# Kernel tuning notes

Measured on AMD Instinct MI355X. Metric: run time of the kernel, lower is better.

Reference implementation:

```python
import jax, jax.numpy as jnp
import numpy as np

HEAD_DIM = 128
NUM_BUCKETS = 32
MAX_DISTANCE = 128


def _rel_pos_bucket(seq_len):
    # T5 causal relative-position bucketing (lucidrains flash-pytorch version)
    pos = jnp.arange(seq_len)
    rel = pos[None, :] - pos[:, None]          # k_pos - q_pos
    n = jnp.maximum(-rel, 0)                   # causal: only past distances
    max_exact = NUM_BUCKETS // 2
    is_small = n < max_exact
    n_safe = jnp.maximum(n, 1).astype(jnp.float32)
    val_large = max_exact + (
        jnp.log(n_safe / max_exact) / np.log(MAX_DISTANCE / max_exact)
        * (NUM_BUCKETS - max_exact)
    ).astype(jnp.int32)
    val_large = jnp.minimum(val_large, NUM_BUCKETS - 1)
    return jnp.where(is_small, n, val_large)   # (S, S) int32


def setup_inputs() -> dict:
    key = jax.random.key(0)
    ks = jax.random.split(key, 10)
    B, S, D, I = 4, 2048, 768, 1536
    s = 0.02
    return {
        "x": jax.random.normal(ks[0], (B, S, D), jnp.float32),
        "v_W": jax.random.normal(ks[1], (D, I), jnp.float32) * s,
        "v_b": jnp.zeros((I,), jnp.float32),
        "g_W": jax.random.normal(ks[2], (D, I), jnp.float32) * s,
        "g_b": jnp.zeros((I,), jnp.float32),
        "in_W": jax.random.normal(ks[3], (D, HEAD_DIM), jnp.float32) * s,
        "in_b": jnp.zeros((HEAD_DIM,), jnp.float32),
        "q_gamma": jax.random.normal(ks[4], (HEAD_DIM,), jnp.float32) * s,
        "q_beta": jnp.zeros((HEAD_DIM,), jnp.float32),
        "k_gamma": jax.random.normal(ks[5], (HEAD_DIM,), jnp.float32) * s,
        "k_beta": jnp.zeros((HEAD_DIM,), jnp.float32),
        "out_W": jax.random.normal(ks[6], (I, D), jnp.float32) * s,
        "out_b": jnp.zeros((D,), jnp.float32),
        "rel_emb": jax.random.normal(ks[7], (NUM_BUCKETS, 1), jnp.float32) * s,
    }


def reference(x, v_W, v_b, g_W, g_b, in_W, in_b,
              q_gamma, q_beta, k_gamma, k_beta, out_W, out_b, rel_emb):
    silu = jax.nn.silu
    S = x.shape[1]
    v = silu(x @ v_W + v_b)                    # (B, S, I)
    gate = silu(x @ g_W + g_b)                 # (B, S, I)
    base = silu(x @ in_W + in_b)               # (B, S, 128)
    q = base * q_gamma + q_beta
    k = base * k_gamma + k_beta
    # scores scaled by sqrt(v dim) per torch code (v.size(-1) = inner_dim)
    attn = jnp.einsum('bns,bms->bnm', q, k) / jnp.sqrt(jnp.float32(v.shape[-1]))
    bias = rel_emb[_rel_pos_bucket(S), 0] * np.sqrt(HEAD_DIM)  # (S, S)
    attn = attn + bias
    causal = jnp.triu(jnp.ones((S, S), bool), 1)
    attn = jnp.where(causal, 0.0, attn)        # masked_fill to 0 before relu^2
    attn = jnp.square(jax.nn.relu(attn))       # ReLU^2 attention (no softmax)
    o = jnp.einsum('bnm,bme->bne', attn, v) * gate
    return o @ out_W + out_b                   # (B, S, D)
```

## Files before the change

### kernel.cpp

```cpp
#include <hip/hip_runtime.h>


typedef short short8 __attribute__((ext_vector_type(8)));
typedef float f32x4 __attribute__((ext_vector_type(4)));
typedef unsigned short us4 __attribute__((ext_vector_type(4)));
typedef float fl4 __attribute__((ext_vector_type(4)));

#define BM 128
#define BN 128
#define BK 64

enum { EPI_VT = 0, EPI_GQK = 1, EPI_SCORES = 3, EPI_OUT = 5 };

__device__ __forceinline__ unsigned short f2bf(float f) {
  unsigned u = __builtin_bit_cast(unsigned, f);
  u += 0x7FFFu + ((u >> 16) & 1u);
  return (unsigned short)(u >> 16);
}
__device__ __forceinline__ float bf2f(unsigned short b) {
  return __builtin_bit_cast(float, ((unsigned)b) << 16);
}
__device__ __forceinline__ float silu_f(float x) { return x / (1.0f + __expf(-x)); }

__device__ __forceinline__ void gl_lds(const unsigned short* gp, unsigned short* lp) {
  __builtin_amdgcn_global_load_lds((const __attribute__((address_space(1))) void*)gp,
                                   (__attribute__((address_space(3))) void*)lp, 16, 0, 0);
}

__device__ __forceinline__ void stage_tile(const unsigned short* __restrict__ g,
                                           int row_stride, int r0, int ko,
                                           unsigned short* lds, int w, int l) {
#pragma unroll
  for (int c = 0; c < 4; ++c) {
    int e = ((w * 4 + c) << 9) + l * 8;
    int row = e >> 6;
    int kk = e & 63;
    gl_lds(g + (size_t)(r0 + row) * row_stride + (ko + kk), lds + e);
  }
}

template <int EPI>
__global__ __launch_bounds__(256) void gemm_k(
    const unsigned short* __restrict__ A,
    const unsigned short* __restrict__ Bt,
    char* __restrict__ out0, char* __restrict__ out1, char* __restrict__ out2,
    const float* __restrict__ f0, const float* __restrict__ f1,
    const float* __restrict__ f2, const float* __restrict__ f3,
    const float* __restrict__ f4, const float* __restrict__ f5,
    const unsigned short* __restrict__ A2,
    const float* __restrict__ bias_tab,
    int K, long long az, long long btz, long long ozb) {
  __shared__ unsigned short As[BM * BK];
  __shared__ unsigned short Bs[BN * BK];

  const int t = threadIdx.x;
  const int l = t & 63;
  const int w = t >> 6;
  const int z = blockIdx.z;

  bool qk = false;
  int m0, n0;
  if constexpr (EPI == EPI_SCORES) {
    int ti = blockIdx.x;
    int r = (int)((sqrtf((float)(8 * ti + 1)) - 1.0f) * 0.5f);
    if ((r + 1) * (r + 2) / 2 <= ti) ++r;
    int c = ti - r * (r + 1) / 2;
    m0 = c * BM;
    n0 = r * BN;
  } else if constexpr (EPI == EPI_GQK) {
    qk = (blockIdx.y == 12);
    if (qk) A = A2;
    m0 = qk ? 0 : blockIdx.y * BM;
    n0 = blockIdx.x * BN;
  } else {
    m0 = blockIdx.y * BM;
    n0 = blockIdx.x * BN;
  }

  A += (size_t)z * az;
  Bt += (size_t)z * btz;
  out0 += (size_t)z * ozb;

  const int wm = (w >> 1) * 64;
  const int wn = (w & 1) * 64;
  const int quad = l >> 4;
  const int lr = quad * 4;
  const int lc = l & 15;

  f32x4 acc[4][4] = {};

  for (int ko = 0; ko < K; ko += BK) {
    stage_tile(A, K, m0, ko, As, w, l);
    stage_tile(Bt, K, n0, ko, Bs, w, l);
    __syncthreads();
#pragma unroll
    for (int kk = 0; kk < 2; ++kk) {
      short8 af[4], bfr[4];
#pragma unroll
      for (int i = 0; i < 4; ++i)
        af[i] = *(const short8*)&As[(wm + i * 16 + lc) * BK + kk * 32 + quad * 8];
#pragma unroll
      for (int j = 0; j < 4; ++j)
        bfr[j] = *(const short8*)&Bs[(wn + j * 16 + lc) * BK + kk * 32 + quad * 8];
#pragma unroll
      for (int i = 0; i < 4; ++i)
#pragma unroll
        for (int j = 0; j < 4; ++j)
          acc[i][j] = __builtin_amdgcn_mfma_f32_16x16x32_bf16(af[i], bfr[j], acc[i][j], 0, 0, 0);
    }
    __syncthreads();
  }

#pragma unroll
  for (int i = 0; i < 4; ++i) {
    const int gm = m0 + wm + i * 16 + lr;
#pragma unroll
    for (int j = 0; j < 4; ++j) {
      const int gn = n0 + wn + j * 16 + lc;
      f32x4 a = acc[i][j];
      if constexpr (EPI == EPI_VT) {
        float bn_ = f0[gn];
        us4 pk;
#pragma unroll
        for (int r = 0; r < 4; ++r) pk[r] = f2bf(silu_f(a[r] + bn_));
        size_t off = (size_t)(gm >> 11) * (1536 * 2048) + (size_t)gn * 2048 + (gm & 2047);
        *(us4*)((unsigned short*)out0 + off) = pk;
      } else if constexpr (EPI == EPI_GQK) {
        if (!qk) {
          fl4 bv = *(const fl4*)&f0[gm];
          us4 pk;
#pragma unroll
          for (int r = 0; r < 4; ++r) pk[r] = f2bf(silu_f(a[r] + bv[r]));
          *(us4*)((unsigned short*)out0 + (size_t)gn * 1536 + gm) = pk;
        } else {
          fl4 bb = *(const fl4*)&f1[gm];
          fl4 qg = *(const fl4*)&f2[gm];
          fl4 qb = *(const fl4*)&f3[gm];
          fl4 kg = *(const fl4*)&f4[gm];
          fl4 kb = *(const fl4*)&f5[gm];
          us4 pq, pk2;
#pragma unroll
          for (int r = 0; r < 4; ++r) {
            float s = silu_f(a[r] + bb[r]);
            pq[r] = f2bf(s * qg[r] + qb[r]);
            pk2[r] = f2bf(s * kg[r] + kb[r]);
          }
          *(us4*)((unsigned short*)out1 + (size_t)gn * 128 + gm) = pq;
          *(us4*)((unsigned short*)out2 + (size_t)gn * 128 + gm) = pk2;
        }
      } else if constexpr (EPI == EPI_SCORES) {
        const float SCALE = 0.025515518153991442f;
        us4 pk;
#pragma unroll
        for (int r = 0; r < 4; ++r) {
          int mm = gm + r;
          float v = 0.0f;
          if (mm <= gn) {
            float tt = fmaf(a[r], SCALE, bias_tab[gn - mm]);
            tt = fmaxf(tt, 0.0f);
            v = tt * tt;
          }
          pk[r] = f2bf(v);
        }
        *(us4*)((unsigned short*)out0 + (size_t)gn * 2048 + gm) = pk;
      } else {
        fl4 ob = *(const fl4*)&f0[gm];
        fl4 res;
#pragma unroll
        for (int r = 0; r < 4; ++r) res[r] = a[r] + ob[r];
        *(fl4*)((float*)out0 + (size_t)gn * 768 + gm) = res;
      }
    }
  }
}

__global__ __launch_bounds__(256) void gemm_og(
    const unsigned short* __restrict__ Vt,
    const unsigned short* __restrict__ P,
    const unsigned short* __restrict__ gate,
    unsigned short* __restrict__ og) {
  __shared__ unsigned short As[64 * 64];
  __shared__ unsigned short Bs[128 * 64];
  const int t = threadIdx.x, l = t & 63, w = t >> 6;
  const int pair = blockIdx.x;
  const int m0 = blockIdx.y * 64;
  const int z = blockIdx.z;
  const unsigned short* A = Vt + (size_t)z * 1536 * 2048;
  const unsigned short* B = P + (size_t)z * 2048 * 2048;
  const unsigned short* G = gate + (size_t)z * 2048 * 1536;
  unsigned short* O = og + (size_t)z * 2048 * 1536;
  const int wm = (w >> 1) * 32, wn = (w & 1) * 64;
  const int quad = l >> 4, lr = quad * 4, lc = l & 15;

#pragma unroll
  for (int pass = 0; pass < 2; ++pass) {
    const int nt = pass ? 15 - pair : pair;
    const int n0 = nt * 128;
    const int kend = n0 + 128;
    f32x4 acc[2][4] = {};
    for (int ko = 0; ko < kend; ko += 64) {
#pragma unroll
      for (int c = 0; c < 2; ++c) {
        int e = ((w * 2 + c) << 9) + l * 8;
        gl_lds(A + (size_t)(m0 + (e >> 6)) * 2048 + ko + (e & 63), As + e);
      }
#pragma unroll
      for (int c = 0; c < 4; ++c) {
        int e = ((w * 4 + c) << 9) + l * 8;
        gl_lds(B + (size_t)(n0 + (e >> 6)) * 2048 + ko + (e & 63), Bs + e);
      }
      __syncthreads();
#pragma unroll
      for (int kk = 0; kk < 2; ++kk) {
        short8 af[2], bfr[4];
#pragma unroll
        for (int i = 0; i < 2; ++i)
          af[i] = *(const short8*)&As[(wm + i * 16 + lc) * 64 + kk * 32 + quad * 8];
#pragma unroll
        for (int j = 0; j < 4; ++j)
          bfr[j] = *(const short8*)&Bs[(wn + j * 16 + lc) * 64 + kk * 32 + quad * 8];
#pragma unroll
        for (int i = 0; i < 2; ++i)
#pragma unroll
          for (int j = 0; j < 4; ++j)
            acc[i][j] = __builtin_amdgcn_mfma_f32_16x16x32_bf16(af[i], bfr[j], acc[i][j], 0, 0, 0);
      }
      __syncthreads();
    }
#pragma unroll
    for (int i = 0; i < 2; ++i) {
      const int gm = m0 + wm + i * 16 + lr;
#pragma unroll
      for (int j = 0; j < 4; ++j) {
        const int gn = n0 + wn + j * 16 + lc;
        us4 g4 = *(const us4*)&G[(size_t)gn * 1536 + gm];
        us4 pk;
#pragma unroll
        for (int r = 0; r < 4; ++r) pk[r] = f2bf(acc[i][j][r] * bf2f(g4[r]));
        *(us4*)&O[(size_t)gn * 1536 + gm] = pk;
      }
    }
  }
}

__global__ void cvt_bf16(const float* __restrict__ in, unsigned short* __restrict__ out, int n) {
  int i = (blockIdx.x * blockDim.x + threadIdx.x) * 4;
  if (i < n) {
    fl4 v = *(const fl4*)&in[i];
    us4 o;
#pragma unroll
    for (int r = 0; r < 4; ++r) o[r] = f2bf(v[r]);
    *(us4*)&out[i] = o;
  }
}

__global__ void transpose_cvt4(const float* __restrict__ s0, unsigned short* __restrict__ d0,
                               const float* __restrict__ s1, unsigned short* __restrict__ d1,
                               const float* __restrict__ s2, unsigned short* __restrict__ d2,
                               const float* __restrict__ s3, unsigned short* __restrict__ d3) {
  __shared__ float tile[32][33];
  const float* in;
  unsigned short* out;
  int K_, N_, bxm, bym;
  switch (blockIdx.z) {
    case 0: in = s0; out = d0; K_ = 768; N_ = 1536; bxm = 48; bym = 24; break;
    case 1: in = s1; out = d1; K_ = 768; N_ = 1536; bxm = 48; bym = 24; break;
    case 2: in = s2; out = d2; K_ = 768; N_ = 128;  bxm = 4;  bym = 24; break;
    default: in = s3; out = d3; K_ = 1536; N_ = 768; bxm = 24; bym = 48; break;
  }
  if ((int)blockIdx.x >= bxm || (int)blockIdx.y >= bym) return;
  int bn = blockIdx.x * 32, bk = blockIdx.y * 32;
  int tx = threadIdx.x, ty = threadIdx.y;
#pragma unroll
  for (int i2 = 0; i2 < 32; i2 += 8)
    tile[ty + i2][tx] = in[(size_t)(bk + ty + i2) * N_ + (bn + tx)];
  __syncthreads();
#pragma unroll
  for (int i2 = 0; i2 < 32; i2 += 8)
    out[(size_t)(bn + ty + i2) * K_ + (bk + tx)] = f2bf(tile[tx][ty + i2]);
}

__global__ void build_bias(const float* __restrict__ rel_emb, float* __restrict__ tab) {
  int d = blockIdx.x * blockDim.x + threadIdx.x;
  if (d < 2048) {
    int bucket;
    if (d < 16) {
      bucket = d;
    } else {
      float n = (float)d;
      int vl = 16 + (int)((logf(n * 0.0625f) / logf(8.0f)) * 16.0f);
      bucket = vl < 31 ? vl : 31;
    }
    tab[d] = rel_emb[bucket] * 11.3137085f;
  }
}

extern "C" void kernel_launch(void* const* d_in, const int* in_sizes, int n_in,
                              void* d_out, int out_size, void* d_ws, size_t ws_size,
                              hipStream_t stream) {
  const float* x    = (const float*)d_in[0];
  const float* vW   = (const float*)d_in[1];
  const float* v_b  = (const float*)d_in[2];
  const float* gW   = (const float*)d_in[3];
  const float* g_b  = (const float*)d_in[4];
  const float* inW  = (const float*)d_in[5];
  const float* in_b = (const float*)d_in[6];
  const float* q_g  = (const float*)d_in[7];
  const float* q_be = (const float*)d_in[8];
  const float* k_g  = (const float*)d_in[9];
  const float* k_be = (const float*)d_in[10];
  const float* oW   = (const float*)d_in[11];
  const float* o_b  = (const float*)d_in[12];
  const float* rel  = (const float*)d_in[13];

  char* p = (char*)d_ws;
  auto alloc = [&](size_t bytes) -> char* {
    char* r = p;
    p += (bytes + 255) & ~(size_t)255;
    return r;
  };
  unsigned short* x_bf = (unsigned short*)alloc(8192ull * 768 * 2);
  unsigned short* vWt  = (unsigned short*)alloc(1536ull * 768 * 2);
  unsigned short* gWt  = (unsigned short*)alloc(1536ull * 768 * 2);
  unsigned short* inWt = (unsigned short*)alloc(128ull * 768 * 2);
  unsigned short* oWt  = (unsigned short*)alloc(768ull * 1536 * 2);
  unsigned short* wq   = (unsigned short*)alloc(8192ull * 128 * 2);
  unsigned short* wk   = (unsigned short*)alloc(8192ull * 128 * 2);
  unsigned short* vt   = (unsigned short*)alloc(4ull * 1536 * 2048 * 2);
  unsigned short* gate = (unsigned short*)alloc(8192ull * 1536 * 2);
  unsigned short* P    = (unsigned short*)alloc(4ull * 2048 * 2048 * 2);
  unsigned short* og   = (unsigned short*)alloc(8192ull * 1536 * 2);
  float* btab          = (float*)alloc(2048 * 4);

  cvt_bf16<<<dim3(6144), dim3(256), 0, stream>>>(x, x_bf, 8192 * 768);
  transpose_cvt4<<<dim3(48, 48, 4), dim3(32, 8), 0, stream>>>(vW, vWt, gW, gWt, inW, inWt, oW, oWt);
  build_bias<<<dim3(8), dim3(256), 0, stream>>>(rel, btab);

  gemm_k<EPI_VT><<<dim3(12, 64, 1), 256, 0, stream>>>(
      x_bf, vWt, (char*)vt, nullptr, nullptr, v_b, nullptr, nullptr, nullptr, nullptr,
      nullptr, nullptr, nullptr, 768, 0, 0, 0);
  gemm_k<EPI_GQK><<<dim3(64, 13, 1), 256, 0, stream>>>(
      gWt, x_bf, (char*)gate, (char*)wq, (char*)wk, g_b, in_b, q_g, q_be, k_g, k_be,
      inWt, nullptr, 768, 0, 0, 0);
  gemm_k<EPI_SCORES><<<dim3(136, 1, 4), 256, 0, stream>>>(
      wk, wq, (char*)P, nullptr, nullptr, nullptr, nullptr, nullptr, nullptr, nullptr, nullptr,
      nullptr, btab, 128, 2048ll * 128, 2048ll * 128, 2048ll * 2048 * 2);
  gemm_og<<<dim3(8, 24, 4), 256, 0, stream>>>(vt, P, gate, og);
  gemm_k<EPI_OUT><<<dim3(64, 6, 1), 256, 0, stream>>>(
      oWt, og, (char*)d_out, nullptr, nullptr, o_b, nullptr, nullptr, nullptr, nullptr, nullptr,
      nullptr, nullptr, 1536, 0, 0, 0);
}
```

Measured before the change: 337.0 us.

## Fuse input projections into one GEMM, retile og kernel, add XCD-aware block mapping

The v, gate and q/k projections become a single GEMM over a stacked weight matrix, so x is streamed once per tile and two launches collapse into one. The gate output is now stored transposed. The og kernel moves from 64-row tiles with paired passes to 128x128 tiles, with a block-id mapping that orders causal work longest-first and spreads it across XCDs. The output GEMM also gets XCD-aware block swizzling. The risks are uncoalesced scalar stores for wq/wk and strided scalar gate loads in the og epilogue, and the og kernel loses the pairing that balanced its triangular work.

```diff
diff --git a/kernel.cpp b/kernel.cpp
--- a/kernel.cpp
+++ b/kernel.cpp
@@ -6,12 +6,6 @@
 typedef unsigned short us4 __attribute__((ext_vector_type(4)));
 typedef float fl4 __attribute__((ext_vector_type(4)));
 
-#define BM 128
-#define BN 128
-#define BK 64
-
-enum { EPI_VT = 0, EPI_GQK = 1, EPI_SCORES = 3, EPI_OUT = 5 };
-
 __device__ __forceinline__ unsigned short f2bf(float f) {
   unsigned u = __builtin_bit_cast(unsigned, f);
   u += 0x7FFFu + ((u >> 16) & 1u);
@@ -33,81 +27,56 @@
 #pragma unroll
   for (int c = 0; c < 4; ++c) {
     int e = ((w * 4 + c) << 9) + l * 8;
-    int row = e >> 6;
-    int kk = e & 63;
-    gl_lds(g + (size_t)(r0 + row) * row_stride + (ko + kk), lds + e);
-  }
-}
-
-template <int EPI>
-__global__ __launch_bounds__(256) void gemm_k(
-    const unsigned short* __restrict__ A,
-    const unsigned short* __restrict__ Bt,
-    char* __restrict__ out0, char* __restrict__ out1, char* __restrict__ out2,
-    const float* __restrict__ f0, const float* __restrict__ f1,
-    const float* __restrict__ f2, const float* __restrict__ f3,
-    const float* __restrict__ f4, const float* __restrict__ f5,
-    const unsigned short* __restrict__ A2,
-    const float* __restrict__ bias_tab,
-    int K, long long az, long long btz, long long ozb) {
-  __shared__ unsigned short As[BM * BK];
-  __shared__ unsigned short Bs[BN * BK];
-
-  const int t = threadIdx.x;
-  const int l = t & 63;
-  const int w = t >> 6;
-  const int z = blockIdx.z;
-
-  bool qk = false;
-  int m0, n0;
-  if constexpr (EPI == EPI_SCORES) {
-    int ti = blockIdx.x;
-    int r = (int)((sqrtf((float)(8 * ti + 1)) - 1.0f) * 0.5f);
-    if ((r + 1) * (r + 2) / 2 <= ti) ++r;
-    int c = ti - r * (r + 1) / 2;
-    m0 = c * BM;
-    n0 = r * BN;
-  } else if constexpr (EPI == EPI_GQK) {
-    qk = (blockIdx.y == 12);
-    if (qk) A = A2;
-    m0 = qk ? 0 : blockIdx.y * BM;
-    n0 = blockIdx.x * BN;
-  } else {
-    m0 = blockIdx.y * BM;
-    n0 = blockIdx.x * BN;
-  }
-
-  A += (size_t)z * az;
-  Bt += (size_t)z * btz;
-  out0 += (size_t)z * ozb;
-
-  const int wm = (w >> 1) * 64;
-  const int wn = (w & 1) * 64;
-  const int quad = l >> 4;
-  const int lr = quad * 4;
-  const int lc = l & 15;
+    gl_lds(g + (size_t)(r0 + (e >> 6)) * row_stride + (ko + (e & 63)), lds + e);
+  }
+}
+
+__device__ __forceinline__ void mfma_step(const unsigned short* As, const unsigned short* Bs,
+                                          f32x4 acc[4][4], int wm, int wn, int quad, int lc) {
+#pragma unroll
+  for (int kk = 0; kk < 2; ++kk) {
+    short8 af[4], bfr[4];
+#pragma unroll
+    for (int i = 0; i < 4; ++i)
+      af[i] = *(const short8*)&As[(wm + i * 16 + lc) * 64 + kk * 32 + quad * 8];
+#pragma unroll
+    for (int j = 0; j < 4; ++j)
+      bfr[j] = *(const short8*)&Bs[(wn + j * 16 + lc) * 64 + kk * 32 + quad * 8];
+#pragma unroll
+    for (int i = 0; i < 4; ++i)
+#pragma unroll
+      for (int j = 0; j < 4; ++j)
+        acc[i][j] = __builtin_amdgcn_mfma_f32_16x16x32_bf16(af[i], bfr[j], acc[i][j], 0, 0, 0);
+  }
+}
+
+__global__ __launch_bounds__(256) void g123_k(
+    const unsigned short* __restrict__ X,
+    const unsigned short* __restrict__ Wst,
+    unsigned short* __restrict__ vt,
+    unsigned short* __restrict__ gateT,
+    unsigned short* __restrict__ wq,
+    unsigned short* __restrict__ wk,
+    const float* __restrict__ v_b, const float* __restrict__ g_b,
+    const float* __restrict__ in_b, const float* __restrict__ q_g,
+    const float* __restrict__ q_be, const float* __restrict__ k_g,
+    const float* __restrict__ k_be) {
+  __shared__ unsigned short As[128 * 64];
+  __shared__ unsigned short Bs[128 * 64];
+  const int t = threadIdx.x, l = t & 63, w = t >> 6;
+  const int id = blockIdx.x;
+  const int xcd = id & 7, rest = id >> 3;
+  const int n = rest % 25, m = (rest / 25) * 8 + xcd;
+  const int m0 = m * 128, n0 = n * 128;
+  const int wm = (w >> 1) * 64, wn = (w & 1) * 64;
+  const int quad = l >> 4, lr = quad * 4, lc = l & 15;
 
   f32x4 acc[4][4] = {};
-
-  for (int ko = 0; ko < K; ko += BK) {
-    stage_tile(A, K, m0, ko, As, w, l);
-    stage_tile(Bt, K, n0, ko, Bs, w, l);
-    __syncthreads();
-#pragma unroll
-    for (int kk = 0; kk < 2; ++kk) {
-      short8 af[4], bfr[4];
-#pragma unroll
-      for (int i = 0; i < 4; ++i)
-        af[i] = *(const short8*)&As[(wm + i * 16 + lc) * BK + kk * 32 + quad * 8];
-#pragma unroll
-      for (int j = 0; j < 4; ++j)
-        bfr[j] = *(const short8*)&Bs[(wn + j * 16 + lc) * BK + kk * 32 + quad * 8];
-#pragma unroll
-      for (int i = 0; i < 4; ++i)
-#pragma unroll
-        for (int j = 0; j < 4; ++j)
-          acc[i][j] = __builtin_amdgcn_mfma_f32_16x16x32_bf16(af[i], bfr[j], acc[i][j], 0, 0, 0);
-    }
+  for (int ko = 0; ko < 768; ko += 64) {
+    stage_tile(X, 768, m0, ko, As, w, l);
+    stage_tile(Wst, 768, n0, ko, Bs, w, l);
+    __syncthreads();
+    mfma_step(As, Bs, acc, wm, wn, quad, lc);
     __syncthreads();
   }
 
@@ -118,127 +87,162 @@
     for (int j = 0; j < 4; ++j) {
       const int gn = n0 + wn + j * 16 + lc;
       f32x4 a = acc[i][j];
-      if constexpr (EPI == EPI_VT) {
-        float bn_ = f0[gn];
+      if (n0 < 1536) {
+        float bv = v_b[gn];
         us4 pk;
 #pragma unroll
-        for (int r = 0; r < 4; ++r) pk[r] = f2bf(silu_f(a[r] + bn_));
+        for (int r = 0; r < 4; ++r) pk[r] = f2bf(silu_f(a[r] + bv));
         size_t off = (size_t)(gm >> 11) * (1536 * 2048) + (size_t)gn * 2048 + (gm & 2047);
-        *(us4*)((unsigned short*)out0 + off) = pk;
-      } else if constexpr (EPI == EPI_GQK) {
-        if (!qk) {
-          fl4 bv = *(const fl4*)&f0[gm];
-          us4 pk;
-#pragma unroll
-          for (int r = 0; r < 4; ++r) pk[r] = f2bf(silu_f(a[r] + bv[r]));
-          *(us4*)((unsigned short*)out0 + (size_t)gn * 1536 + gm) = pk;
-        } else {
-          fl4 bb = *(const fl4*)&f1[gm];
-          fl4 qg = *(const fl4*)&f2[gm];
-          fl4 qb = *(const fl4*)&f3[gm];
-          fl4 kg = *(const fl4*)&f4[gm];
-          fl4 kb = *(const fl4*)&f5[gm];
-          us4 pq, pk2;
-#pragma unroll
-          for (int r = 0; r < 4; ++r) {
-            float s = silu_f(a[r] + bb[r]);
-            pq[r] = f2bf(s * qg[r] + qb[r]);
-            pk2[r] = f2bf(s * kg[r] + kb[r]);
-          }
-          *(us4*)((unsigned short*)out1 + (size_t)gn * 128 + gm) = pq;
-          *(us4*)((unsigned short*)out2 + (size_t)gn * 128 + gm) = pk2;
+        *(us4*)&vt[off] = pk;
+      } else if (n0 < 3072) {
+        float bv = g_b[gn - 1536];
+        us4 pk;
+#pragma unroll
+        for (int r = 0; r < 4; ++r) pk[r] = f2bf(silu_f(a[r] + bv));
+        *(us4*)&gateT[(size_t)(gn - 1536) * 8192 + gm] = pk;
+      } else {
+        int h = gn - 3072;
+        float bb = in_b[h], qg = q_g[h], qb = q_be[h], kg = k_g[h], kb = k_be[h];
+#pragma unroll
+        for (int r = 0; r < 4; ++r) {
+          float s = silu_f(a[r] + bb);
+          wq[(size_t)(gm + r) * 128 + h] = f2bf(s * qg + qb);
+          wk[(size_t)(gm + r) * 128 + h] = f2bf(s * kg + kb);
         }
-      } else if constexpr (EPI == EPI_SCORES) {
-        const float SCALE = 0.025515518153991442f;
-        us4 pk;
-#pragma unroll
-        for (int r = 0; r < 4; ++r) {
-          int mm = gm + r;
-          float v = 0.0f;
-          if (mm <= gn) {
-            float tt = fmaf(a[r], SCALE, bias_tab[gn - mm]);
-            tt = fmaxf(tt, 0.0f);
-            v = tt * tt;
-          }
-          pk[r] = f2bf(v);
+      }
+    }
+  }
+}
+
+__global__ __launch_bounds__(256) void scores_k(
+    const unsigned short* __restrict__ wk, const unsigned short* __restrict__ wq,
+    unsigned short* __restrict__ P, const float* __restrict__ btab) {
+  __shared__ unsigned short As[128 * 64];
+  __shared__ unsigned short Bs[128 * 64];
+  const int t = threadIdx.x, l = t & 63, w = t >> 6;
+  const int z = blockIdx.z;
+  int ti = blockIdx.x;
+  int r = (int)((sqrtf((float)(8 * ti + 1)) - 1.0f) * 0.5f);
+  if ((r + 1) * (r + 2) / 2 <= ti) ++r;
+  int c = ti - r * (r + 1) / 2;
+  const int m0 = c * 128, n0 = r * 128;
+  const unsigned short* A = wk + (size_t)z * 2048 * 128;
+  const unsigned short* Bt = wq + (size_t)z * 2048 * 128;
+  unsigned short* Pz = P + (size_t)z * 2048 * 2048;
+  const int wm = (w >> 1) * 64, wn = (w & 1) * 64;
+  const int quad = l >> 4, lr = quad * 4, lc = l & 15;
+
+  f32x4 acc[4][4] = {};
+  for (int ko = 0; ko < 128; ko += 64) {
+    stage_tile(A, 128, m0, ko, As, w, l);
+    stage_tile(Bt, 128, n0, ko, Bs, w, l);
+    __syncthreads();
+    mfma_step(As, Bs, acc, wm, wn, quad, lc);
+    __syncthreads();
+  }
+  const float SCALE = 0.025515518153991442f;
+#pragma unroll
+  for (int i = 0; i < 4; ++i) {
+    const int gm = m0 + wm + i * 16 + lr;
+#pragma unroll
+    for (int j = 0; j < 4; ++j) {
+      const int gn = n0 + wn + j * 16 + lc;
+      us4 pk;
+#pragma unroll
+      for (int r2 = 0; r2 < 4; ++r2) {
+        int mm = gm + r2;
+        float v = 0.0f;
+        if (mm <= gn) {
+          float tt = fmaf(acc[i][j][r2], SCALE, btab[gn - mm]);
+          tt = fmaxf(tt, 0.0f);
+          v = tt * tt;
         }
-        *(us4*)((unsigned short*)out0 + (size_t)gn * 2048 + gm) = pk;
-      } else {
-        fl4 ob = *(const fl4*)&f0[gm];
-        fl4 res;
-#pragma unroll
-        for (int r = 0; r < 4; ++r) res[r] = a[r] + ob[r];
-        *(fl4*)((float*)out0 + (size_t)gn * 768 + gm) = res;
+        pk[r2] = f2bf(v);
       }
-    }
-  }
-}
-
-__global__ __launch_bounds__(256) void gemm_og(
+      *(us4*)&Pz[(size_t)gn * 2048 + gm] = pk;
+    }
+  }
+}
+
+__global__ __launch_bounds__(256) void og_k(
     const unsigned short* __restrict__ Vt,
     const unsigned short* __restrict__ P,
-    const unsigned short* __restrict__ gate,
+    const unsigned short* __restrict__ gateT,
     unsigned short* __restrict__ og) {
-  __shared__ unsigned short As[64 * 64];
+  __shared__ unsigned short As[128 * 64];
   __shared__ unsigned short Bs[128 * 64];
   const int t = threadIdx.x, l = t & 63, w = t >> 6;
-  const int pair = blockIdx.x;
-  const int m0 = blockIdx.y * 64;
-  const int z = blockIdx.z;
+  const int id = blockIdx.x;
+  const int bblk = id / 96, rr = id % 96;
+  const int xcd = rr & 7, mi = rr >> 3;
+  const int half = xcd >> 2, z = xcd & 3;
+  const int nt = 15 - 2 * bblk - (half ^ (bblk & 1));
+  const int m0 = mi * 128;
+  const int n0 = nt * 128;
+  const int kend = n0 + 128;
   const unsigned short* A = Vt + (size_t)z * 1536 * 2048;
   const unsigned short* B = P + (size_t)z * 2048 * 2048;
-  const unsigned short* G = gate + (size_t)z * 2048 * 1536;
-  unsigned short* O = og + (size_t)z * 2048 * 1536;
-  const int wm = (w >> 1) * 32, wn = (w & 1) * 64;
+  const int wm = (w >> 1) * 64, wn = (w & 1) * 64;
   const int quad = l >> 4, lr = quad * 4, lc = l & 15;
 
-#pragma unroll
-  for (int pass = 0; pass < 2; ++pass) {
-    const int nt = pass ? 15 - pair : pair;
-    const int n0 = nt * 128;
-    const int kend = n0 + 128;
-    f32x4 acc[2][4] = {};
-    for (int ko = 0; ko < kend; ko += 64) {
-#pragma unroll
-      for (int c = 0; c < 2; ++c) {
-        int e = ((w * 2 + c) << 9) + l * 8;
-        gl_lds(A + (size_t)(m0 + (e >> 6)) * 2048 + ko + (e & 63), As + e);
+  f32x4 acc[4][4] = {};
+  for (int ko = 0; ko < kend; ko += 64) {
+    stage_tile(A, 2048, m0, ko, As, w, l);
+    stage_tile(B, 2048, n0, ko, Bs, w, l);
+    __syncthreads();
+    mfma_step(As, Bs, acc, wm, wn, quad, lc);
+    __syncthreads();
+  }
+#pragma unroll
+  for (int i = 0; i < 4; ++i) {
+    const int gm = m0 + wm + i * 16 + lr;
+#pragma unroll
+    for (int j = 0; j < 4; ++j) {
+      const int gn = n0 + wn + j * 16 + lc;
+      us4 pk;
+#pragma unroll
+      for (int r2 = 0; r2 < 4; ++r2) {
+        float g = bf2f(gateT[(size_t)(gm + r2) * 8192 + z * 2048 + gn]);
+        pk[r2] = f2bf(acc[i][j][r2] * g);
       }
-#pragma unroll
-      for (int c = 0; c < 4; ++c) {
-        int e = ((w * 4 + c) << 9) + l * 8;
-        gl_lds(B + (size_t)(n0 + (e >> 6)) * 2048 + ko + (e & 63), Bs + e);
-      }
-      __syncthreads();
-#pragma unroll
-      for (int kk = 0; kk < 2; ++kk) {
-        short8 af[2], bfr[4];
-#pragma unroll
-        for (int i = 0; i < 2; ++i)
-          af[i] = *(const short8*)&As[(wm + i * 16 + lc) * 64 + kk * 32 + quad * 8];
-#pragma unroll
-        for (int j = 0; j < 4; ++j)
-          bfr[j] = *(const short8*)&Bs[(wn + j * 16 + lc) * 64 + kk * 32 + quad * 8];
-#pragma unroll
-        for (int i = 0; i < 2; ++i)
-#pragma unroll
-          for (int j = 0; j < 4; ++j)
-            acc[i][j] = __builtin_amdgcn_mfma_f32_16x16x32_bf16(af[i], bfr[j], acc[i][j], 0, 0, 0);
-      }
-      __syncthreads();
-    }
-#pragma unroll
-    for (int i = 0; i < 2; ++i) {
-      const int gm = m0 + wm + i * 16 + lr;
-#pragma unroll
-      for (int j = 0; j < 4; ++j) {
-        const int gn = n0 + wn + j * 16 + lc;
-        us4 g4 = *(const us4*)&G[(size_t)gn * 1536 + gm];
-        us4 pk;
-#pragma unroll
-        for (int r = 0; r < 4; ++r) pk[r] = f2bf(acc[i][j][r] * bf2f(g4[r]));
-        *(us4*)&O[(size_t)gn * 1536 + gm] = pk;
-      }
+      *(us4*)&og[((size_t)z * 2048 + gn) * 1536 + gm] = pk;
+    }
+  }
+}
+
+__global__ __launch_bounds__(256) void gout_k(
+    const unsigned short* __restrict__ A,
+    const unsigned short* __restrict__ Bt,
+    float* __restrict__ out, const float* __restrict__ o_b) {
+  __shared__ unsigned short As[128 * 64];
+  __shared__ unsigned short Bs[128 * 64];
+  const int t = threadIdx.x, l = t & 63, w = t >> 6;
+  const int id = blockIdx.x;
+  const int xcd = id & 7, rest = id >> 3;
+  const int m = rest % 6, n = (rest / 6) * 8 + xcd;
+  const int m0 = m * 128, n0 = n * 128;
+  const int wm = (w >> 1) * 64, wn = (w & 1) * 64;
+  const int quad = l >> 4, lr = quad * 4, lc = l & 15;
+
+  f32x4 acc[4][4] = {};
+  for (int ko = 0; ko < 1536; ko += 64) {
+    stage_tile(A, 1536, m0, ko, As, w, l);
+    stage_tile(Bt, 1536, n0, ko, Bs, w, l);
+    __syncthreads();
+    mfma_step(As, Bs, acc, wm, wn, quad, lc);
+    __syncthreads();
+  }
+#pragma unroll
+  for (int i = 0; i < 4; ++i) {
+    const int gm = m0 + wm + i * 16 + lr;
+#pragma unroll
+    for (int j = 0; j < 4; ++j) {
+      const int gn = n0 + wn + j * 16 + lc;
+      fl4 ob = *(const fl4*)&o_b[gm];
+      fl4 res;
+#pragma unroll
+      for (int r2 = 0; r2 < 4; ++r2) res[r2] = acc[i][j][r2] + ob[r2];
+      *(fl4*)&out[(size_t)gn * 768 + gm] = res;
     }
   }
 }
@@ -319,15 +323,16 @@
     p += (bytes + 255) & ~(size_t)255;
     return r;
   };
-  unsigned short* x_bf = (unsigned short*)alloc(8192ull * 768 * 2);
-  unsigned short* vWt  = (unsigned short*)alloc(1536ull * 768 * 2);
-  unsigned short* gWt  = (unsigned short*)alloc(1536ull * 768 * 2);
-  unsigned short* inWt = (unsigned short*)alloc(128ull * 768 * 2);
+  unsigned short* x_bf   = (unsigned short*)alloc(8192ull * 768 * 2);
+  unsigned short* wstack = (unsigned short*)alloc(3200ull * 768 * 2);
+  unsigned short* vWt  = wstack;
+  unsigned short* gWt  = wstack + 1536ull * 768;
+  unsigned short* inWt = wstack + 3072ull * 768;
   unsigned short* oWt  = (unsigned short*)alloc(768ull * 1536 * 2);
   unsigned short* wq   = (unsigned short*)alloc(8192ull * 128 * 2);
   unsigned short* wk   = (unsigned short*)alloc(8192ull * 128 * 2);
   unsigned short* vt   = (unsigned short*)alloc(4ull * 1536 * 2048 * 2);
-  unsigned short* gate = (unsigned short*)alloc(8192ull * 1536 * 2);
+  unsigned short* gateT= (unsigned short*)alloc(1536ull * 8192 * 2);
   unsigned short* P    = (unsigned short*)alloc(4ull * 2048 * 2048 * 2);
   unsigned short* og   = (unsigned short*)alloc(8192ull * 1536 * 2);
   float* btab          = (float*)alloc(2048 * 4);
@@ -336,17 +341,9 @@
   transpose_cvt4<<<dim3(48, 48, 4), dim3(32, 8), 0, stream>>>(vW, vWt, gW, gWt, inW, inWt, oW, oWt);
   build_bias<<<dim3(8), dim3(256), 0, stream>>>(rel, btab);
 
-  gemm_k<EPI_VT><<<dim3(12, 64, 1), 256, 0, stream>>>(
-      x_bf, vWt, (char*)vt, nullptr, nullptr, v_b, nullptr, nullptr, nullptr, nullptr,
-      nullptr, nullptr, nullptr, 768, 0, 0, 0);
-  gemm_k<EPI_GQK><<<dim3(64, 13, 1), 256, 0, stream>>>(
-      gWt, x_bf, (char*)gate, (char*)wq, (char*)wk, g_b, in_b, q_g, q_be, k_g, k_be,
-      inWt, nullptr, 768, 0, 0, 0);
-  gemm_k<EPI_SCORES><<<dim3(136, 1, 4), 256, 0, stream>>>(
-      wk, wq, (char*)P, nullptr, nullptr, nullptr, nullptr, nullptr, nullptr, nullptr, nullptr,
-      nullptr, btab, 128, 2048ll * 128, 2048ll * 128, 2048ll * 2048 * 2);
-  gemm_og<<<dim3(8, 24, 4), 256, 0, stream>>>(vt, P, gate, og);
-  gemm_k<EPI_OUT><<<dim3(64, 6, 1), 256, 0, stream>>>(
-      oWt, og, (char*)d_out, nullptr, nullptr, o_b, nullptr, nullptr, nullptr, nullptr, nullptr,
-      nullptr, nullptr, 1536, 0, 0, 0);
-}
+  g123_k<<<dim3(1600), 256, 0, stream>>>(x_bf, wstack, vt, gateT, wq, wk,
+                                         v_b, g_b, in_b, q_g, q_be, k_g, k_be);
+  scores_k<<<dim3(136, 1, 4), 256, 0, stream>>>(wk, wq, P, btab);
+  og_k<<<dim3(768), 256, 0, stream>>>(vt, P, gateT, og);
+  gout_k<<<dim3(384), 256, 0, stream>>>(oWt, og, (float*)d_out, o_b);
+}
```

Result: faster. 319.6 us (-5.2%).
